# Kernel optimization log

Measured on AMD Instinct MI355X. Metric: run time of the kernel, lower is better.

Reference implementation:

```python
import jax, jax.numpy as jnp
import numpy as np

PRUNE_RATIO = 0.5
NOISE_SCALE = 0.1
MIXUP_ALPHA = 0.05
TEMPERATURE = 0.5
B, N, D = 32, 4096, 256


def setup_inputs() -> dict:
    key = jax.random.key(0)
    k1, k2, k3 = jax.random.split(key, 3)
    seq = jax.random.normal(k1, (B, N, D), dtype=jnp.float32)
    attn_weights = jax.random.uniform(k2, (B, N), dtype=jnp.float32)
    uniform_noise = jax.random.uniform(k3, (B, N), dtype=jnp.float32)
    return {"seq": seq, "attn_weights": attn_weights, "uniform_noise": uniform_noise}


def reference(seq, attn_weights, uniform_noise):
    b, n, d = seq.shape
    k = max(1, int(n * (1.0 - PRUNE_RATIO)))
    # training branch: gumbel noise from the provided uniform draw
    gumbel = -jnp.log(-jnp.log(uniform_noise + 1e-10) + 1e-10)
    noisy = attn_weights + NOISE_SCALE * gumbel                      # (B, N)
    soft = jax.nn.softmax(noisy / TEMPERATURE, axis=-1)              # (B, N)
    _, top_idx = jax.lax.top_k(soft, k)                              # (B, K) int32
    # gather selected tokens: (B, K, D)
    selected = jnp.take_along_axis(seq, top_idx[:, :, None], axis=1)
    # mixup: mean of the pruned (non-selected) tokens
    mask = jnp.ones((b, n), dtype=seq.dtype).at[
        jnp.arange(b)[:, None], top_idx
    ].set(0.0)                                                       # (B, N), 1 on pruned
    remaining_sum = jnp.einsum('bn,bnd->bd', mask, seq)              # (B, D)
    remaining_count = mask.sum(axis=1, keepdims=True) + 1e-10        # (B, 1)
    remaining_mean = remaining_sum / remaining_count                 # (B, D)
    return selected + MIXUP_ALPHA * remaining_mean[:, None, :]       # (B, K, D)
```

## Files before the change

### kernel.cpp

```cpp
#include <hip/hip_runtime.h>

#define B_ 32
#define N_ 4096
#define D_ 256
#define K_ 2048

#define ISPLIT 2
#define JSPLIT 8
#define EPT 8
#define JSLICE (N_ / JSPLIT)

__global__ __launch_bounds__(256) void key_kernel(
    const float* __restrict__ attn, const float* __restrict__ noise,
    unsigned long long* __restrict__ keys,
    unsigned long long* __restrict__ rankBuf64,
    float* __restrict__ meanAccum) {
  const int t = blockIdx.x * 256 + threadIdx.x;
  float u = noise[t];
  float a = attn[t];
  float x = __fadd_rn(u, 1e-10f);
  float l1 = (float)log((double)x);
  float inner = __fadd_rn(-l1, 1e-10f);
  float g = -(float)log((double)inner);
  float noisy = __fadd_rn(a, __fmul_rn(0.1f, g));
  unsigned int fb = __float_as_uint(noisy);
  fb = (fb & 0x80000000u) ? ~fb : (fb | 0x80000000u);
  int i = t & (N_ - 1);
  keys[t] = ((unsigned long long)fb << 32) | (unsigned int)(~i);
  if (t < B_ * N_ / 4) rankBuf64[t] = 0ull;
  if (t < B_ * D_) meanAccum[t] = 0.0f;
}

__global__ __launch_bounds__(256) void rank_kernel(
    const unsigned long long* __restrict__ keys,
    unsigned long long* __restrict__ rankBuf64) {
  const int b = blockIdx.y;
  const int ic = blockIdx.x >> 3;
  const int jc = blockIdx.x & (JSPLIT - 1);
  __shared__ __align__(16) ulonglong2 lk2[JSLICE / 2];

  const unsigned long long* __restrict__ bk = keys + (size_t)b * N_;

  const ulonglong2* __restrict__ gk2 = (const ulonglong2*)(bk + jc * JSLICE);
  lk2[threadIdx.x] = gk2[threadIdx.x];

  const int ibase = ic * (N_ / ISPLIT) + threadIdx.x * EPT;
  unsigned long long ki[EPT];
  const ulonglong2* __restrict__ gi2 = (const ulonglong2*)(bk + ibase);
#pragma unroll
  for (int e2 = 0; e2 < EPT / 2; ++e2) {
    ulonglong2 v = gi2[e2];
    ki[2 * e2] = v.x;
    ki[2 * e2 + 1] = v.y;
  }
  __syncthreads();

  unsigned int rk[EPT] = {0u, 0u, 0u, 0u, 0u, 0u, 0u, 0u};
#pragma unroll 4
  for (int j = 0; j < JSLICE / 2; ++j) {
    ulonglong2 v = lk2[j];
#pragma unroll
    for (int e = 0; e < EPT; ++e) {
      rk[e] += (v.x > ki[e]);
      rk[e] += (v.y > ki[e]);
    }
  }

  unsigned long long p0 =
      (unsigned long long)rk[0] | ((unsigned long long)rk[1] << 16) |
      ((unsigned long long)rk[2] << 32) | ((unsigned long long)rk[3] << 48);
  unsigned long long p1 =
      (unsigned long long)rk[4] | ((unsigned long long)rk[5] << 16) |
      ((unsigned long long)rk[6] << 32) | ((unsigned long long)rk[7] << 48);
  const size_t q = ((size_t)b * N_ + ibase) >> 2;
  atomicAdd(&rankBuf64[q], p0);
  atomicAdd(&rankBuf64[q + 1], p1);
}

__global__ __launch_bounds__(256) void scatter_mean_kernel(
    const unsigned short* __restrict__ rankBuf16, const float* __restrict__ seq,
    int* __restrict__ sortedIdx, float* __restrict__ meanAccum) {
  const int b = blockIdx.y;
  const int i = blockIdx.x * 256 + threadIdx.x;
  const unsigned int rank = rankBuf16[(size_t)b * N_ + i];
  sortedIdx[(size_t)b * N_ + rank] = i;

  __shared__ int plist[256];
  __shared__ int pcount;
  if (threadIdx.x == 0) pcount = 0;
  __syncthreads();
  if (rank >= K_) {
    int slot = atomicAdd(&pcount, 1);
    plist[slot] = i;
  }
  __syncthreads();
  const int cnt = pcount;

  const int dv = threadIdx.x & 63;
  const int sub = threadIdx.x >> 6;
  float4 acc = make_float4(0.f, 0.f, 0.f, 0.f);
  for (int r = sub; r < cnt; r += 4) {
    const float4* row = (const float4*)(seq + ((size_t)b * N_ + plist[r]) * D_);
    float4 v = row[dv];
    acc.x += v.x; acc.y += v.y; acc.z += v.z; acc.w += v.w;
  }

  __shared__ float4 red[4][64];
  red[sub][dv] = acc;
  __syncthreads();
  if (sub == 0) {
    float4 s0 = red[0][dv], s1 = red[1][dv], s2 = red[2][dv], s3 = red[3][dv];
    float sx = s0.x + s1.x + s2.x + s3.x;
    float sy = s0.y + s1.y + s2.y + s3.y;
    float sz = s0.z + s1.z + s2.z + s3.z;
    float sw = s0.w + s1.w + s2.w + s3.w;
    float* dst = meanAccum + b * D_ + dv * 4;
    atomicAdd(dst + 0, sx);
    atomicAdd(dst + 1, sy);
    atomicAdd(dst + 2, sz);
    atomicAdd(dst + 3, sw);
  }
}

__global__ __launch_bounds__(256) void out_kernel(
    const float* __restrict__ seq, const int* __restrict__ sortedIdx,
    const float* __restrict__ meanAccum, float* __restrict__ out) {
  const unsigned int t = blockIdx.x * 256u + threadIdx.x;
  const int dv = t & 63;
  const int j = (t >> 6) & (K_ - 1);
  const int b = t >> 17;

  int idx = sortedIdx[b * N_ + j];
  float4 v = ((const float4*)(seq + ((size_t)b * N_ + idx) * D_))[dv];
  float4 m = ((const float4*)(meanAccum + b * D_))[dv];
  const float inv_cnt = 1.0f / 2048.0f;
  float4 o;
  o.x = v.x + 0.05f * (m.x * inv_cnt);
  o.y = v.y + 0.05f * (m.y * inv_cnt);
  o.z = v.z + 0.05f * (m.z * inv_cnt);
  o.w = v.w + 0.05f * (m.w * inv_cnt);
  ((float4*)out)[t] = o;
}

extern "C" void kernel_launch(void* const* d_in, const int* in_sizes, int n_in,
                              void* d_out, int out_size, void* d_ws, size_t ws_size,
                              hipStream_t stream) {
  const float* seq  = (const float*)d_in[0];
  const float* attn = (const float*)d_in[1];
  const float* nois = (const float*)d_in[2];
  float* out = (float*)d_out;

  int* sortedIdx   = (int*)d_ws;
  float* meanAccum = (float*)((char*)d_ws + (size_t)B_ * N_ * 4);
  unsigned long long* keys =
      (unsigned long long*)((char*)d_ws + (size_t)B_ * N_ * 4 + (size_t)B_ * D_ * 4);
  unsigned long long* rankBuf64 =
      (unsigned long long*)((char*)keys + (size_t)B_ * N_ * 8);
  unsigned short* rankBuf16 = (unsigned short*)rankBuf64;

  key_kernel<<<(B_ * N_) / 256, 256, 0, stream>>>(attn, nois, keys, rankBuf64, meanAccum);
  rank_kernel<<<dim3(ISPLIT * JSPLIT, B_), 256, 0, stream>>>(keys, rankBuf64);
  scatter_mean_kernel<<<dim3(N_ / 256, B_), 256, 0, stream>>>(rankBuf16, seq, sortedIdx, meanAccum);
  const int total4 = B_ * K_ * (D_ / 4);
  out_kernel<<<total4 / 256, 256, 0, stream>>>(seq, sortedIdx, meanAccum, out);
}
```

Before: 265.1 us.

## Drop sorted index buffer, scatter selected rows by rank and split rank work finer

The rank kernel now splits the comparison range into twice as many slices, so it launches more blocks. Each block does a shorter inner loop, and more packed atomics are added. The scatter of sorted indices is removed. The output kernel compacts selected tokens per 128-token chunk and writes each row straight to its rank position, while the mean kernel handles pruned tokens in 128-token chunks with more blocks. This removes the sortedIdx write and the dependent indirect read, in exchange for scattered output writes and lower thread utilisation in the compaction phase.

Result: no change. 261.9 us (-1.2%).

```diff
diff --git a/kernel.cpp b/kernel.cpp
--- a/kernel.cpp
+++ b/kernel.cpp
@@ -6,7 +6,7 @@
 #define K_ 2048
 
 #define ISPLIT 2
-#define JSPLIT 8
+#define JSPLIT 16
 #define EPT 8
 #define JSLICE (N_ / JSPLIT)
 
@@ -35,14 +35,13 @@
     const unsigned long long* __restrict__ keys,
     unsigned long long* __restrict__ rankBuf64) {
   const int b = blockIdx.y;
-  const int ic = blockIdx.x >> 3;
+  const int ic = blockIdx.x >> 4;
   const int jc = blockIdx.x & (JSPLIT - 1);
-  __shared__ __align__(16) ulonglong2 lk2[JSLICE / 2];
+  __shared__ __align__(16) unsigned long long lk[JSLICE];
 
   const unsigned long long* __restrict__ bk = keys + (size_t)b * N_;
 
-  const ulonglong2* __restrict__ gk2 = (const ulonglong2*)(bk + jc * JSLICE);
-  lk2[threadIdx.x] = gk2[threadIdx.x];
+  lk[threadIdx.x] = bk[jc * JSLICE + threadIdx.x];
 
   const int ibase = ic * (N_ / ISPLIT) + threadIdx.x * EPT;
   unsigned long long ki[EPT];
@@ -55,6 +54,7 @@
   }
   __syncthreads();
 
+  const ulonglong2* lk2 = (const ulonglong2*)lk;
   unsigned int rk[EPT] = {0u, 0u, 0u, 0u, 0u, 0u, 0u, 0u};
 #pragma unroll 4
   for (int j = 0; j < JSLICE / 2; ++j) {
@@ -77,21 +77,22 @@
   atomicAdd(&rankBuf64[q + 1], p1);
 }
 
-__global__ __launch_bounds__(256) void scatter_mean_kernel(
+__global__ __launch_bounds__(256) void mean_kernel(
     const unsigned short* __restrict__ rankBuf16, const float* __restrict__ seq,
-    int* __restrict__ sortedIdx, float* __restrict__ meanAccum) {
+    float* __restrict__ meanAccum) {
   const int b = blockIdx.y;
-  const int i = blockIdx.x * 256 + threadIdx.x;
-  const unsigned int rank = rankBuf16[(size_t)b * N_ + i];
-  sortedIdx[(size_t)b * N_ + rank] = i;
-
-  __shared__ int plist[256];
+  const int ibase = blockIdx.x * 128;
+  __shared__ int plist[128];
   __shared__ int pcount;
   if (threadIdx.x == 0) pcount = 0;
   __syncthreads();
-  if (rank >= K_) {
-    int slot = atomicAdd(&pcount, 1);
-    plist[slot] = i;
+  if (threadIdx.x < 128) {
+    const int i = ibase + threadIdx.x;
+    const unsigned int rank = rankBuf16[(size_t)b * N_ + i];
+    if (rank >= K_) {
+      int slot = atomicAdd(&pcount, 1);
+      plist[slot] = i;
+    }
   }
   __syncthreads();
   const int cnt = pcount;
@@ -123,23 +124,41 @@
 }
 
 __global__ __launch_bounds__(256) void out_kernel(
-    const float* __restrict__ seq, const int* __restrict__ sortedIdx,
+    const unsigned short* __restrict__ rankBuf16, const float* __restrict__ seq,
     const float* __restrict__ meanAccum, float* __restrict__ out) {
-  const unsigned int t = blockIdx.x * 256u + threadIdx.x;
-  const int dv = t & 63;
-  const int j = (t >> 6) & (K_ - 1);
-  const int b = t >> 17;
+  const int b = blockIdx.y;
+  const int ibase = blockIdx.x * 128;
+  __shared__ int pl_i[128];
+  __shared__ unsigned short pl_r[128];
+  __shared__ int pcount;
+  if (threadIdx.x == 0) pcount = 0;
+  __syncthreads();
+  if (threadIdx.x < 128) {
+    const int i = ibase + threadIdx.x;
+    const unsigned int rank = rankBuf16[(size_t)b * N_ + i];
+    if (rank < K_) {
+      int slot = atomicAdd(&pcount, 1);
+      pl_i[slot] = i;
+      pl_r[slot] = (unsigned short)rank;
+    }
+  }
+  __syncthreads();
+  const int cnt = pcount;
 
-  int idx = sortedIdx[b * N_ + j];
-  float4 v = ((const float4*)(seq + ((size_t)b * N_ + idx) * D_))[dv];
+  const int dv = threadIdx.x & 63;
+  const int sub = threadIdx.x >> 6;
   float4 m = ((const float4*)(meanAccum + b * D_))[dv];
-  const float inv_cnt = 1.0f / 2048.0f;
-  float4 o;
-  o.x = v.x + 0.05f * (m.x * inv_cnt);
-  o.y = v.y + 0.05f * (m.y * inv_cnt);
-  o.z = v.z + 0.05f * (m.z * inv_cnt);
-  o.w = v.w + 0.05f * (m.w * inv_cnt);
-  ((float4*)out)[t] = o;
+  const float s = 0.05f * (1.0f / 2048.0f);
+  float4 mix;
+  mix.x = m.x * s; mix.y = m.y * s; mix.z = m.z * s; mix.w = m.w * s;
+
+  for (int r = sub; r < cnt; r += 4) {
+    const float4* row = (const float4*)(seq + ((size_t)b * N_ + pl_i[r]) * D_);
+    float4 v = row[dv];
+    float4 o;
+    o.x = v.x + mix.x; o.y = v.y + mix.y; o.z = v.z + mix.z; o.w = v.w + mix.w;
+    ((float4*)(out + ((size_t)b * K_ + pl_r[r]) * D_))[dv] = o;
+  }
 }
 
 extern "C" void kernel_launch(void* const* d_in, const int* in_sizes, int n_in,
@@ -150,17 +169,15 @@
   const float* nois = (const float*)d_in[2];
   float* out = (float*)d_out;
 
-  int* sortedIdx   = (int*)d_ws;
-  float* meanAccum = (float*)((char*)d_ws + (size_t)B_ * N_ * 4);
+  float* meanAccum = (float*)d_ws;
   unsigned long long* keys =
-      (unsigned long long*)((char*)d_ws + (size_t)B_ * N_ * 4 + (size_t)B_ * D_ * 4);
+      (unsigned long long*)((char*)d_ws + (size_t)B_ * D_ * 4);
   unsigned long long* rankBuf64 =
       (unsigned long long*)((char*)keys + (size_t)B_ * N_ * 8);
   unsigned short* rankBuf16 = (unsigned short*)rankBuf64;
 
   key_kernel<<<(B_ * N_) / 256, 256, 0, stream>>>(attn, nois, keys, rankBuf64, meanAccum);
   rank_kernel<<<dim3(ISPLIT * JSPLIT, B_), 256, 0, stream>>>(keys, rankBuf64);
-  scatter_mean_kernel<<<dim3(N_ / 256, B_), 256, 0, stream>>>(rankBuf16, seq, sortedIdx, meanAccum);
-  const int total4 = B_ * K_ * (D_ / 4);
-  out_kernel<<<total4 / 256, 256, 0, stream>>>(seq, sortedIdx, meanAccum, out);
+  mean_kernel<<<dim3(32, B_), 256, 0, stream>>>(rankBuf16, seq, meanAccum);
+  out_kernel<<<dim3(32, B_), 256, 0, stream>>>(rankBuf16, seq, meanAccum, out);
 }
```
